# Kernel tuning notes

Measured on AMD Instinct MI355X. Metric: run time of the kernel, lower is better.

Reference implementation:

```python
import jax, jax.numpy as jnp
import numpy as np

B, N, D_V, D_H, D_K = 1024, 131072, 256, 256, 256


def setup_inputs() -> dict:
    key = jax.random.key(0)
    ks = jax.random.split(key, 12)
    s = 0.02
    V = jax.random.normal(ks[0], (B, D_V), dtype=jnp.float32)
    H = jax.random.normal(ks[1], (N, D_H), dtype=jnp.float32)
    batch_idx = jnp.sort(jax.random.randint(ks[2], (N,), 0, B)).astype(jnp.int32)
    Wq = jax.random.normal(ks[3], (D_K, D_V), dtype=jnp.float32) / np.sqrt(D_V)
    bq = jnp.zeros((D_K,), dtype=jnp.float32)
    Wk = jax.random.normal(ks[4], (D_K, D_H), dtype=jnp.float32) / np.sqrt(D_H)
    bk = jnp.zeros((D_K,), dtype=jnp.float32)
    Wv = jax.random.normal(ks[5], (D_V, D_H), dtype=jnp.float32) / np.sqrt(D_H)
    bv = jnp.zeros((D_V,), dtype=jnp.float32)
    Wo = jax.random.normal(ks[6], (D_V, 2 * D_V), dtype=jnp.float32) / np.sqrt(2 * D_V)
    bo = jnp.zeros((D_V,), dtype=jnp.float32)
    return {"V": V, "H": H, "batch_idx": batch_idx,
            "Wq": Wq, "bq": bq, "Wk": Wk, "bk": bk,
            "Wv": Wv, "bv": bv, "Wo": Wo, "bo": bo}


def reference(V, H, batch_idx, Wq, bq, Wk, bk, Wv, bv, Wo, bo):
    nb = V.shape[0]
    Q = V @ Wq.T + bq            # [B, d_k] one query per graph
    K = H @ Wk.T + bk            # [N, d_k]
    Vval = H @ Wv.T + bv         # [N, d_v]
    scale = 1.0 / jnp.sqrt(jnp.asarray(K.shape[-1], K.dtype))
    # ragged attention scores: each node attends to its graph's query
    scores = jnp.einsum('nd,nd->n', K, Q[batch_idx]) * scale   # [N]
    m = jax.ops.segment_max(scores, batch_idx, num_segments=nb)  # [B]
    e = jnp.exp(scores - m[batch_idx])
    denom = jax.ops.segment_sum(e, batch_idx, num_segments=nb)   # [B]
    attn = e / denom[batch_idx]                                  # [N]
    H_tilde = jax.ops.segment_sum(attn[:, None] * Vval, batch_idx, num_segments=nb)  # [B, d_v]
    U = jnp.concatenate([V, H_tilde], axis=-1)                   # [B, 2*d_v]
    out = U @ Wo.T + bo                                          # [B, d_v]
    # graphs with zero nodes pass V through unchanged
    count = jax.ops.segment_sum(jnp.ones_like(scores), batch_idx, num_segments=nb)
    return jnp.where((count > 0)[:, None], out, V)
```

## Files before the change

kernel.cpp:

```cpp
#include <hip/hip_runtime.h>
#include <math.h>

#define D 256
#define TWOD 512
#define BB 1024
#define NN 131072
#define LOG2E 1.4426950408889634f

typedef float v4f __attribute__((ext_vector_type(4)));

__device__ __forceinline__ v4f ldg_nt(const float* p, bool valid) {
  v4f z = {0.f, 0.f, 0.f, 0.f};
  if (valid) z = __builtin_nontemporal_load((const v4f*)p);
  return z;
}

__device__ __forceinline__ float dot4(v4f a, v4f b) {
  return fmaf(a.w, b.w, fmaf(a.z, b.z, fmaf(a.y, b.y, a.x * b.x)));
}

__global__ __launch_bounds__(256) void prep_kernel(
    const float* __restrict__ Wq, const float* __restrict__ bq,
    const float* __restrict__ Wk, const float* __restrict__ Wv,
    const float* __restrict__ bv, const float* __restrict__ Wo,
    const float* __restrict__ bo, const int* __restrict__ bidx,
    float* __restrict__ Mt, float* __restrict__ WfT,
    float* __restrict__ bqt, float* __restrict__ cvec,
    int* __restrict__ offs) {
  const int blk = blockIdx.x;
  const int t = threadIdx.x;
  if (blk < 64) {
    __shared__ __align__(16) float part[4][4][D];
    const int wq = t >> 6, lane = t & 63;
    const int d0 = blk * 4;
    v4f a0 = {0.f, 0.f, 0.f, 0.f}, a1 = a0, a2 = a0, a3 = a0;
    for (int ee = 0; ee < 64; ++ee) {
      const int e = wq * 64 + ee;
      const v4f wk4 = *(const v4f*)&Wk[(size_t)e * D + lane * 4];
      const float* wqr = Wq + (size_t)e * D + d0;
      a0 += wk4 * wqr[0];
      a1 += wk4 * wqr[1];
      a2 += wk4 * wqr[2];
      a3 += wk4 * wqr[3];
    }
    *(v4f*)&part[wq][0][lane * 4] = a0;
    *(v4f*)&part[wq][1][lane * 4] = a1;
    *(v4f*)&part[wq][2][lane * 4] = a2;
    *(v4f*)&part[wq][3][lane * 4] = a3;
    __syncthreads();
    #pragma unroll
    for (int r = 0; r < 4; ++r)
      Mt[(size_t)(d0 + r) * D + t] =
          part[0][r][t] + part[1][r][t] + part[2][r][t] + part[3][r][t];
  } else if (blk < 128) {
    const int h0 = (blk - 64) * 4;
    float a0 = 0.f, a1 = 0.f, a2 = 0.f, a3 = 0.f;
    for (int v = 0; v < D; ++v) {
      const float wo = Wo[(size_t)t * TWOD + D + v];
      const float* wvr = Wv + (size_t)v * D + h0;
      a0 = fmaf(wvr[0], wo, a0);
      a1 = fmaf(wvr[1], wo, a1);
      a2 = fmaf(wvr[2], wo, a2);
      a3 = fmaf(wvr[3], wo, a3);
    }
    WfT[(size_t)(D + h0 + 0) * D + t] = a0;
    WfT[(size_t)(D + h0 + 1) * D + t] = a1;
    WfT[(size_t)(D + h0 + 2) * D + t] = a2;
    WfT[(size_t)(D + h0 + 3) * D + t] = a3;
  } else if (blk < 144) {
    __shared__ float tile[64][65];
    const int b = blk - 128;
    const int r0 = (b >> 2) * 64, c0 = (b & 3) * 64;
    const int lane = t & 63, sr = t >> 6;
    #pragma unroll 4
    for (int rr = 0; rr < 16; ++rr) {
      const int r = rr * 4 + sr;
      tile[r][lane] = Wo[(size_t)(r0 + r) * TWOD + c0 + lane];
    }
    __syncthreads();
    #pragma unroll 4
    for (int rr = 0; rr < 16; ++rr) {
      const int r = rr * 4 + sr;
      WfT[(size_t)(c0 + r) * D + r0 + lane] = tile[lane][r];
    }
  } else if (blk == 144) {
    float a = 0.f;
    for (int e = 0; e < D; ++e)
      a = fmaf(Wk[(size_t)e * D + t], bq[e], a);
    bqt[t] = a;
  } else if (blk == 145) {
    float a = bo[t];
    for (int v = 0; v < D; ++v)
      a = fmaf(Wo[(size_t)t * TWOD + D + v], bv[v], a);
    cvec[t] = a;
  } else {
    const int i = (blk - 146) * 256 + t;
    if (i >= NN) return;
    const int b1 = bidx[i];
    const int b2 = (i + 1 < NN) ? bidx[i + 1] : BB;
    if (i == 0) {
      for (int b = 0; b <= b1; ++b) offs[b] = 0;
    }
    for (int b = b1 + 1; b <= b2; ++b) offs[b] = i + 1;
  }
}

__global__ __launch_bounds__(1024) void f_kernel(
    const float* __restrict__ H, const float* __restrict__ V,
    const float* __restrict__ Mt, const float* __restrict__ bqt,
    const int* __restrict__ offs, const float* __restrict__ WfT,
    const float* __restrict__ cvec, float* __restrict__ out) {
  __shared__ __align__(16) char smem[32768 + 4096 + 8192];
  float (*partq)[4][D] = (float(*)[4][D])smem;
  float (*ss)[D] = (float(*)[D])smem;
  float (*part)[4][D] = (float(*)[4][D])smem;
  float* Vs  = (float*)(smem + 32768);
  float* Us2 = (float*)(smem + 36864);
  __shared__ float sm[16], sd[16];
  __shared__ int soff[5];

  const int t = threadIdx.x;
  const int wave = t >> 6, lane = t & 63;
  const int blk = blockIdx.x;
  const int b0 = blk * 4;

  if (t < 5) soff[t] = offs[b0 + t];
  {
    const int i = t >> 8, d = t & 255;
    Vs[i * 256 + d] = V[(size_t)(b0 + i) * D + d];
  }
  __syncthreads();

  const int ib = wave >> 2, ph = wave & 3;
  const int start = soff[ib];
  const int cnt = soff[ib + 1] - start;
  const int ck = (cnt + 3) >> 2;
  const int s0 = start + min(cnt, ph * ck);
  const int e0 = start + min(cnt, (ph + 1) * ck);
  int n = s0;
  v4f c0 = ldg_nt(H + (size_t)n * D + lane * 4, n < e0);
  v4f c1 = ldg_nt(H + (size_t)(n + 1) * D + lane * 4, n + 1 < e0);
  v4f f0 = ldg_nt(H + (size_t)(n + 2) * D + lane * 4, n + 2 < e0);
  v4f f1 = ldg_nt(H + (size_t)(n + 3) * D + lane * 4, n + 3 < e0);

  {
    v4f a0 = {0.f, 0.f, 0.f, 0.f}, a1 = a0, a2 = a0, a3 = a0;
    const int db = wave * 16;
    #pragma unroll 4
    for (int dd = 0; dd < 16; ++dd) {
      const int d = db + dd;
      const v4f w4 = *(const v4f*)(Mt + (size_t)d * D + lane * 4);
      a0 += w4 * Vs[0 * 256 + d];
      a1 += w4 * Vs[1 * 256 + d];
      a2 += w4 * Vs[2 * 256 + d];
      a3 += w4 * Vs[3 * 256 + d];
    }
    if (wave >= 8) {
      *(v4f*)&partq[wave - 8][0][lane * 4] = a0;
      *(v4f*)&partq[wave - 8][1][lane * 4] = a1;
      *(v4f*)&partq[wave - 8][2][lane * 4] = a2;
      *(v4f*)&partq[wave - 8][3][lane * 4] = a3;
    }
    __syncthreads();
    if (wave < 8) {
      v4f p0 = *(const v4f*)&partq[wave][0][lane * 4];
      v4f p1 = *(const v4f*)&partq[wave][1][lane * 4];
      v4f p2 = *(const v4f*)&partq[wave][2][lane * 4];
      v4f p3 = *(const v4f*)&partq[wave][3][lane * 4];
      *(v4f*)&partq[wave][0][lane * 4] = a0 + p0;
      *(v4f*)&partq[wave][1][lane * 4] = a1 + p1;
      *(v4f*)&partq[wave][2][lane * 4] = a2 + p2;
      *(v4f*)&partq[wave][3][lane * 4] = a3 + p3;
    }
  }
  __syncthreads();

  v4f q4 = *(const v4f*)(bqt + lane * 4);
  #pragma unroll
  for (int w = 0; w < 8; ++w) q4 += *(const v4f*)&partq[w][ib][lane * 4];
  __syncthreads();

  float m = -1e30f, den = 0.f;
  v4f acc = {0.f, 0.f, 0.f, 0.f};
  {
    const float SC = 0.0625f * LOG2E;
    const int odd = lane & 1;
    while (n < e0) {
      const int nn = n + 4;
      v4f g0 = ldg_nt(H + (size_t)nn * D + lane * 4, nn < e0);
      v4f g1 = ldg_nt(H + (size_t)(nn + 1) * D + lane * 4, nn + 1 < e0);

      const float d0 = dot4(c0, q4);
      const float d1 = dot4(c1, q4);
      const float mine = odd ? d1 : d0;
      const float oth  = odd ? d0 : d1;
      float s = mine + __shfl_xor(oth, 1);
      s += __shfl_xor(s, 2);
      s += __shfl_xor(s, 4);
      s += __shfl_xor(s, 8);
      s += __shfl_xor(s, 16);
      s += __shfl_xor(s, 32);
      const float sc = (n + odd < e0) ? s * SC : -1e30f;

      const float mm = fmaxf(sc, __shfl_xor(sc, 1));
      const float nm = fmaxf(m, mm);
      const float f = exp2f(m - nm);
      const float w = exp2f(sc - nm);
      const float wx = __shfl_xor(w, 1);
      const float wr0 = odd ? wx : w;
      const float wr1 = odd ? w : wx;
      den = fmaf(den, f, w + wx);
      acc = acc * f + c0 * wr0 + c1 * wr1;
      m = nm;

      c0 = f0; c1 = f1; f0 = g0; f1 = g1; n += 2;
    }
  }
  *(v4f*)&ss[wave][lane * 4] = acc;
  if (lane == 0) { sm[wave] = m; sd[wave] = den; }
  __syncthreads();

  {
    const int i = t >> 8, d = t & 255;
    const int w0 = i * 4;
    const float m0 = sm[w0], m1 = sm[w0 + 1], m2 = sm[w0 + 2], m3 = sm[w0 + 3];
    const float M = fmaxf(fmaxf(m0, m1), fmaxf(m2, m3));
    const float f0m = exp2f(m0 - M), f1m = exp2f(m1 - M);
    const float f2m = exp2f(m2 - M), f3m = exp2f(m3 - M);
    const float Dn = sd[w0] * f0m + sd[w0 + 1] * f1m + sd[w0 + 2] * f2m + sd[w0 + 3] * f3m;
    const float inv = (Dn > 0.f) ? (1.f / Dn) : 0.f;
    const float sv = (ss[w0][d] * f0m + ss[w0 + 1][d] * f1m +
                      ss[w0 + 2][d] * f2m + ss[w0 + 3][d] * f3m) * inv;
    Us2[d * 4 + i] = Vs[i * 256 + d];
    Us2[(D + d) * 4 + i] = sv;
  }
  __syncthreads();

  {
    v4f a0 = {0.f, 0.f, 0.f, 0.f}, a1 = a0, a2 = a0, a3 = a0;
    const int kb = wave * 32;
    #pragma unroll 4
    for (int kk = 0; kk < 32; ++kk) {
      const int k = kb + kk;
      const v4f w4 = *(const v4f*)(WfT + (size_t)k * D + lane * 4);
      const v4f u4 = *(const v4f*)&Us2[k * 4];
      a0 += w4 * u4.x; a1 += w4 * u4.y; a2 += w4 * u4.z; a3 += w4 * u4.w;
    }
    if (wave >= 8) {
      *(v4f*)&part[wave - 8][0][lane * 4] = a0;
      *(v4f*)&part[wave - 8][1][lane * 4] = a1;
      *(v4f*)&part[wave - 8][2][lane * 4] = a2;
      *(v4f*)&part[wave - 8][3][lane * 4] = a3;
    }
    __syncthreads();
    if (wave < 8) {
      v4f p0 = *(const v4f*)&part[wave][0][lane * 4];
      v4f p1 = *(const v4f*)&part[wave][1][lane * 4];
      v4f p2 = *(const v4f*)&part[wave][2][lane * 4];
      v4f p3 = *(const v4f*)&part[wave][3][lane * 4];
      *(v4f*)&part[wave][0][lane * 4] = a0 + p0;
      *(v4f*)&part[wave][1][lane * 4] = a1 + p1;
      *(v4f*)&part[wave][2][lane * 4] = a2 + p2;
      *(v4f*)&part[wave][3][lane * 4] = a3 + p3;
    }
  }
  __syncthreads();
  {
    const int i = t >> 8, d = t & 255;
    const int bb2 = b0 + i;
    float s = cvec[d];
    #pragma unroll
    for (int w = 0; w < 8; ++w) s += part[w][i][d];
    const int c = soff[i + 1] - soff[i];
    out[(size_t)bb2 * D + d] = (c > 0) ? s : Us2[d * 4 + i];
  }
}

extern "C" void kernel_launch(void* const* d_in, const int* in_sizes, int n_in,
                              void* d_out, int out_size, void* d_ws, size_t ws_size,
                              hipStream_t stream) {
  const float* V   = (const float*)d_in[0];
  const float* H   = (const float*)d_in[1];
  const int* bidx  = (const int*)d_in[2];
  const float* Wq  = (const float*)d_in[3];
  const float* bq  = (const float*)d_in[4];
  const float* Wk  = (const float*)d_in[5];
  const float* Wv  = (const float*)d_in[7];
  const float* bv  = (const float*)d_in[8];
  const float* Wo  = (const float*)d_in[9];
  const float* bo  = (const float*)d_in[10];
  float* out = (float*)d_out;

  float* ws  = (float*)d_ws;
  float* Mt  = ws;
  float* WfT = Mt + D * D;
  float* bqt = WfT + TWOD * D;
  float* cv  = bqt + D;
  int* offs  = (int*)(cv + D);

  hipLaunchKernelGGL(prep_kernel, dim3(658), dim3(256), 0, stream,
                     Wq, bq, Wk, Wv, bv, Wo, bo, bidx,
                     Mt, WfT, bqt, cv, offs);
  hipLaunchKernelGGL(f_kernel, dim3(BB / 4), dim3(1024), 0, stream,
                     H, V, Mt, bqt, offs, WfT, cv, out);
}
```

Baseline: 46.79 us.

## Fuse prep and main kernels into one cooperative launch with grid sync

Merges the weight-precompute/offset kernel and the main attention kernel into a single cooperative kernel of 256 blocks of 1024 threads, separated by a grid-wide barrier. The prep work is redistributed across 1024-thread blocks with shared-memory partial reductions, and the offset computation becomes a grid-stride loop. The V tile load is hoisted before the barrier. This removes one kernel launch and the gap between launches, at the cost of grid-sync overhead and cooperative-launch occupancy constraints.

```diff
diff --git a/kernel.cpp b/kernel.cpp
--- a/kernel.cpp
+++ b/kernel.cpp
@@ -1,5 +1,8 @@
 #include <hip/hip_runtime.h>
+#include <hip/hip_cooperative_groups.h>
 #include <math.h>
+
+namespace cg = cooperative_groups;
 
 #define D 256
 #define TWOD 512
@@ -19,116 +22,156 @@
   return fmaf(a.w, b.w, fmaf(a.z, b.z, fmaf(a.y, b.y, a.x * b.x)));
 }
 
-__global__ __launch_bounds__(256) void prep_kernel(
+__global__ __launch_bounds__(1024) void fused_kernel(
+    const float* __restrict__ H, const float* __restrict__ V,
+    const int* __restrict__ bidx,
     const float* __restrict__ Wq, const float* __restrict__ bq,
     const float* __restrict__ Wk, const float* __restrict__ Wv,
     const float* __restrict__ bv, const float* __restrict__ Wo,
-    const float* __restrict__ bo, const int* __restrict__ bidx,
+    const float* __restrict__ bo,
     float* __restrict__ Mt, float* __restrict__ WfT,
     float* __restrict__ bqt, float* __restrict__ cvec,
-    int* __restrict__ offs) {
+    int* __restrict__ offs, float* __restrict__ out) {
+  __shared__ __align__(16) char smem[45056];
+  float (*partq)[4][D] = (float(*)[4][D])smem;
+  float (*ss)[D] = (float(*)[D])smem;
+  float (*part)[4][D] = (float(*)[4][D])smem;
+  float (*jp8)[4][D] = (float(*)[4][D])smem;
+  float (*jp4)[4][D] = (float(*)[4][D])smem;
+  float (*tile)[65] = (float(*)[65])smem;
+  float* spart = (float*)smem;
+  float* Vs  = (float*)(smem + 32768);
+  float* Us2 = (float*)(smem + 36864);
+  __shared__ float sm[16], sd[16];
+  __shared__ int soff[5];
+
+  const int t = threadIdx.x;
+  const int wave = t >> 6, lane = t & 63;
   const int blk = blockIdx.x;
-  const int t = threadIdx.x;
+  const int b0 = blk * 4;
+
+  {
+    const int i = t >> 8, d = t & 255;
+    Vs[i * 256 + d] = V[(size_t)(b0 + i) * D + d];
+  }
+
   if (blk < 64) {
-    __shared__ __align__(16) float part[4][4][D];
-    const int wq = t >> 6, lane = t & 63;
     const int d0 = blk * 4;
+    const int k4 = lane * 4;
     v4f a0 = {0.f, 0.f, 0.f, 0.f}, a1 = a0, a2 = a0, a3 = a0;
-    for (int ee = 0; ee < 64; ++ee) {
-      const int e = wq * 64 + ee;
-      const v4f wk4 = *(const v4f*)&Wk[(size_t)e * D + lane * 4];
+    const int eb = wave * 16;
+    #pragma unroll 4
+    for (int ee = 0; ee < 16; ++ee) {
+      const int e = eb + ee;
+      const v4f wk4 = *(const v4f*)&Wk[(size_t)e * D + k4];
       const float* wqr = Wq + (size_t)e * D + d0;
       a0 += wk4 * wqr[0];
       a1 += wk4 * wqr[1];
       a2 += wk4 * wqr[2];
       a3 += wk4 * wqr[3];
     }
-    *(v4f*)&part[wq][0][lane * 4] = a0;
-    *(v4f*)&part[wq][1][lane * 4] = a1;
-    *(v4f*)&part[wq][2][lane * 4] = a2;
-    *(v4f*)&part[wq][3][lane * 4] = a3;
-    __syncthreads();
-    #pragma unroll
-    for (int r = 0; r < 4; ++r)
-      Mt[(size_t)(d0 + r) * D + t] =
-          part[0][r][t] + part[1][r][t] + part[2][r][t] + part[3][r][t];
+    if (wave >= 8) {
+      *(v4f*)&jp8[wave - 8][0][k4] = a0;
+      *(v4f*)&jp8[wave - 8][1][k4] = a1;
+      *(v4f*)&jp8[wave - 8][2][k4] = a2;
+      *(v4f*)&jp8[wave - 8][3][k4] = a3;
+    }
+    __syncthreads();
+    if (wave < 8) {
+      v4f p0 = *(const v4f*)&jp8[wave][0][k4];
+      v4f p1 = *(const v4f*)&jp8[wave][1][k4];
+      v4f p2 = *(const v4f*)&jp8[wave][2][k4];
+      v4f p3 = *(const v4f*)&jp8[wave][3][k4];
+      *(v4f*)&jp8[wave][0][k4] = a0 + p0;
+      *(v4f*)&jp8[wave][1][k4] = a1 + p1;
+      *(v4f*)&jp8[wave][2][k4] = a2 + p2;
+      *(v4f*)&jp8[wave][3][k4] = a3 + p3;
+    }
+    __syncthreads();
+    {
+      const int r = t >> 8, k = t & 255;
+      float s = 0.f;
+      #pragma unroll
+      for (int w = 0; w < 8; ++w) s += jp8[w][r][k];
+      Mt[(size_t)(d0 + r) * D + k] = s;
+    }
   } else if (blk < 128) {
     const int h0 = (blk - 64) * 4;
+    const int g = t >> 8, d = t & 255;
     float a0 = 0.f, a1 = 0.f, a2 = 0.f, a3 = 0.f;
-    for (int v = 0; v < D; ++v) {
-      const float wo = Wo[(size_t)t * TWOD + D + v];
+    const int vb = g * 64;
+    for (int vv = 0; vv < 64; ++vv) {
+      const int v = vb + vv;
+      const float wo = Wo[(size_t)d * TWOD + D + v];
       const float* wvr = Wv + (size_t)v * D + h0;
       a0 = fmaf(wvr[0], wo, a0);
       a1 = fmaf(wvr[1], wo, a1);
       a2 = fmaf(wvr[2], wo, a2);
       a3 = fmaf(wvr[3], wo, a3);
     }
-    WfT[(size_t)(D + h0 + 0) * D + t] = a0;
-    WfT[(size_t)(D + h0 + 1) * D + t] = a1;
-    WfT[(size_t)(D + h0 + 2) * D + t] = a2;
-    WfT[(size_t)(D + h0 + 3) * D + t] = a3;
+    jp4[g][0][d] = a0; jp4[g][1][d] = a1; jp4[g][2][d] = a2; jp4[g][3][d] = a3;
+    __syncthreads();
+    {
+      const int j = t >> 8, d2 = t & 255;
+      const float s = jp4[0][j][d2] + jp4[1][j][d2] + jp4[2][j][d2] + jp4[3][j][d2];
+      WfT[(size_t)(D + h0 + j) * D + d2] = s;
+    }
   } else if (blk < 144) {
-    __shared__ float tile[64][65];
     const int b = blk - 128;
     const int r0 = (b >> 2) * 64, c0 = (b & 3) * 64;
-    const int lane = t & 63, sr = t >> 6;
-    #pragma unroll 4
-    for (int rr = 0; rr < 16; ++rr) {
-      const int r = rr * 4 + sr;
-      tile[r][lane] = Wo[(size_t)(r0 + r) * TWOD + c0 + lane];
-    }
-    __syncthreads();
-    #pragma unroll 4
-    for (int rr = 0; rr < 16; ++rr) {
-      const int r = rr * 4 + sr;
-      WfT[(size_t)(c0 + r) * D + r0 + lane] = tile[lane][r];
+    const int tl = t & 63, rr = t >> 6;
+    #pragma unroll
+    for (int p = 0; p < 4; ++p) {
+      const int r = p * 16 + rr;
+      tile[r][tl] = Wo[(size_t)(r0 + r) * TWOD + c0 + tl];
+    }
+    __syncthreads();
+    #pragma unroll
+    for (int p = 0; p < 4; ++p) {
+      const int r = p * 16 + rr;
+      WfT[(size_t)(c0 + r) * D + r0 + tl] = tile[tl][r];
     }
   } else if (blk == 144) {
+    const int g = t >> 8, k = t & 255;
     float a = 0.f;
-    for (int e = 0; e < D; ++e)
-      a = fmaf(Wk[(size_t)e * D + t], bq[e], a);
-    bqt[t] = a;
+    const int eb = g * 64;
+    for (int ee = 0; ee < 64; ++ee) {
+      const int e = eb + ee;
+      a = fmaf(Wk[(size_t)e * D + k], bq[e], a);
+    }
+    spart[g * 256 + k] = a;
+    __syncthreads();
+    if (t < 256)
+      bqt[t] = spart[0 * 256 + t] + spart[1 * 256 + t] +
+               spart[2 * 256 + t] + spart[3 * 256 + t];
   } else if (blk == 145) {
-    float a = bo[t];
-    for (int v = 0; v < D; ++v)
-      a = fmaf(Wo[(size_t)t * TWOD + D + v], bv[v], a);
-    cvec[t] = a;
+    const int g = t >> 8, d = t & 255;
+    float a = 0.f;
+    const int vb = g * 64;
+    for (int vv = 0; vv < 64; ++vv) {
+      const int v = vb + vv;
+      a = fmaf(Wo[(size_t)d * TWOD + D + v], bv[v], a);
+    }
+    spart[g * 256 + d] = a;
+    __syncthreads();
+    if (t < 256)
+      cvec[t] = bo[t] + spart[0 * 256 + t] + spart[1 * 256 + t] +
+                spart[2 * 256 + t] + spart[3 * 256 + t];
   } else {
-    const int i = (blk - 146) * 256 + t;
-    if (i >= NN) return;
-    const int b1 = bidx[i];
-    const int b2 = (i + 1 < NN) ? bidx[i + 1] : BB;
-    if (i == 0) {
-      for (int b = 0; b <= b1; ++b) offs[b] = 0;
-    }
-    for (int b = b1 + 1; b <= b2; ++b) offs[b] = i + 1;
-  }
-}
-
-__global__ __launch_bounds__(1024) void f_kernel(
-    const float* __restrict__ H, const float* __restrict__ V,
-    const float* __restrict__ Mt, const float* __restrict__ bqt,
-    const int* __restrict__ offs, const float* __restrict__ WfT,
-    const float* __restrict__ cvec, float* __restrict__ out) {
-  __shared__ __align__(16) char smem[32768 + 4096 + 8192];
-  float (*partq)[4][D] = (float(*)[4][D])smem;
-  float (*ss)[D] = (float(*)[D])smem;
-  float (*part)[4][D] = (float(*)[4][D])smem;
-  float* Vs  = (float*)(smem + 32768);
-  float* Us2 = (float*)(smem + 36864);
-  __shared__ float sm[16], sd[16];
-  __shared__ int soff[5];
-
-  const int t = threadIdx.x;
-  const int wave = t >> 6, lane = t & 63;
-  const int blk = blockIdx.x;
-  const int b0 = blk * 4;
+    const int idx = (blk - 146) * 1024 + t;
+    for (int i = idx; i < NN; i += 110 * 1024) {
+      const int b1 = bidx[i];
+      const int b2 = (i + 1 < NN) ? bidx[i + 1] : BB;
+      if (i == 0) {
+        for (int b = 0; b <= b1; ++b) offs[b] = 0;
+      }
+      for (int b = b1 + 1; b <= b2; ++b) offs[b] = i + 1;
+    }
+  }
+
+  cg::this_grid().sync();
 
   if (t < 5) soff[t] = offs[b0 + t];
-  {
-    const int i = t >> 8, d = t & 255;
-    Vs[i * 256 + d] = V[(size_t)(b0 + i) * D + d];
-  }
   __syncthreads();
 
   const int ib = wave >> 2, ph = wave & 3;
@@ -298,9 +341,11 @@
   float* cv  = bqt + D;
   int* offs  = (int*)(cv + D);
 
-  hipLaunchKernelGGL(prep_kernel, dim3(658), dim3(256), 0, stream,
-                     Wq, bq, Wk, Wv, bv, Wo, bo, bidx,
-                     Mt, WfT, bqt, cv, offs);
-  hipLaunchKernelGGL(f_kernel, dim3(BB / 4), dim3(1024), 0, stream,
-                     H, V, Mt, bqt, offs, WfT, cv, out);
+  void* args[] = {
+      (void*)&H, (void*)&V, (void*)&bidx, (void*)&Wq, (void*)&bq,
+      (void*)&Wk, (void*)&Wv, (void*)&bv, (void*)&Wo, (void*)&bo,
+      (void*)&Mt, (void*)&WfT, (void*)&bqt, (void*)&cv, (void*)&offs,
+      (void*)&out};
+  hipLaunchCooperativeKernel((const void*)fused_kernel, dim3(256), dim3(1024),
+                             args, 0, stream);
 }
```

After: 98.27 us. +110.0%, slower.
